# Kernel tuning notes

Measured on AMD Instinct MI355X. Metric: run time of the kernel, lower is better.

The kernel has to match this reference:

```python
import jax, jax.numpy as jnp
import numpy as np

EMBED_DIM = 1024
NUM_HEADS = 16
HEAD_DIM = EMBED_DIM // NUM_HEADS
SCALE_BASE = EMBED_DIM  # XPOS(head_dim, embed_dim): embed_dim is scale_base
BSZ, SEQ = 8, 1024


def xpos_apply(x, downscale):
    # x: [B*H, L, D]; standard xpos (torchscale) rotary with position-dependent scale
    L, D = x.shape[1], x.shape[2]
    half = D // 2
    s = (jnp.arange(0, D, 2, dtype=jnp.float32) + 0.4 * D) / (1.4 * D)  # [half]
    min_pos = -(L // 2)  # offset = 0
    pos = jnp.arange(min_pos, min_pos + L, dtype=jnp.float32)  # [L]
    scale = s[None, :] ** (pos[:, None] / SCALE_BASE)  # [L, half]
    inv_freq = 1.0 / (10000.0 ** (jnp.arange(half, dtype=jnp.float32) / half))
    sinus = jnp.arange(L, dtype=jnp.float32)[:, None] * inv_freq[None, :]  # [L, half]
    sin, cos = jnp.sin(sinus), jnp.cos(sinus)
    if downscale:
        scale = 1.0 / scale
    # duplicate_interleave: repeat each column twice -> [L, D]
    sin_d = jnp.repeat(sin * scale, 2, axis=-1)
    cos_d = jnp.repeat(cos * scale, 2, axis=-1)
    x1, x2 = x[..., 0::2], x[..., 1::2]
    rot = jnp.stack([-x2, x1], axis=-1).reshape(x.shape)  # rotate_every_two
    return x * cos_d + rot * sin_d


def setup_inputs() -> dict:
    key = jax.random.key(0)
    ks = jax.random.split(key, 12)
    std = 0.02
    inp = {
        'query': jax.random.normal(ks[0], (BSZ, SEQ, EMBED_DIM), jnp.float32),
        'key': jax.random.normal(ks[1], (BSZ, SEQ, EMBED_DIM), jnp.float32),
        'value': jax.random.normal(ks[2], (BSZ, SEQ, EMBED_DIM), jnp.float32),
        'wq': jax.random.normal(ks[3], (EMBED_DIM, EMBED_DIM), jnp.float32) * std,
        'bq': jax.random.normal(ks[4], (EMBED_DIM,), jnp.float32) * std,
        'wk': jax.random.normal(ks[5], (EMBED_DIM, EMBED_DIM), jnp.float32) * std,
        'bk': jax.random.normal(ks[6], (EMBED_DIM,), jnp.float32) * std,
        'wv': jax.random.normal(ks[7], (EMBED_DIM, EMBED_DIM), jnp.float32) * std,
        'bv': jax.random.normal(ks[8], (EMBED_DIM,), jnp.float32) * std,
        'wo': jax.random.normal(ks[9], (EMBED_DIM, EMBED_DIM), jnp.float32) * std,
        'bo': jax.random.normal(ks[10], (EMBED_DIM,), jnp.float32) * std,
    }
    return inp


def reference(query, key, value, wq, bq, wk, bk, wv, bv, wo, bo):
    B, T, E = query.shape
    S = key.shape[1]
    scaling = HEAD_DIM ** -0.5
    q = (query @ wq.T + bq) * scaling
    k = key @ wk.T + bk
    v = value @ wv.T + bv

    def split_heads(x, L):
        return x.reshape(B, L, NUM_HEADS, HEAD_DIM).transpose(0, 2, 1, 3).reshape(B * NUM_HEADS, L, HEAD_DIM)

    q = split_heads(q, T)
    k = split_heads(k, S)
    v = split_heads(v, S)
    k = xpos_apply(k, downscale=True)
    q = xpos_apply(q, downscale=False)
    attn_w = jnp.einsum('btd,bsd->bts', q, k)  # [B*H, T, S]
    attn_w = jax.nn.softmax(attn_w.astype(jnp.float32), axis=-1).astype(q.dtype)
    attn = jnp.einsum('bts,bsd->btd', attn_w, v)  # [B*H, T, D]
    attn = attn.reshape(B, NUM_HEADS, T, HEAD_DIM).transpose(0, 2, 1, 3).reshape(B, T, E)
    return attn @ wo.T + bo
```

## Files before the change

### kernel.cpp

```cpp
#include <hip/hip_runtime.h>


#define BSZ  8
#define SEQ  1024
#define EMB  1024
#define NH   16
#define HD   64
#define HALF 32
#define BH   (BSZ*NH)
#define MROWS (BSZ*SEQ)

typedef __attribute__((ext_vector_type(4))) float f32x4;
typedef __attribute__((ext_vector_type(8))) short bf16x8;

__device__ __forceinline__ ushort f2bf(float f) {
    union { float f; unsigned u; } v; v.f = f;
    return (ushort)((v.u + 0x7FFFu + ((v.u >> 16) & 1u)) >> 16);
}

__device__ __forceinline__ void async16(void* lds, const void* g) {
    __builtin_amdgcn_global_load_lds(
        (const __attribute__((address_space(1))) unsigned int*)g,
        (__attribute__((address_space(3))) unsigned int*)lds, 16, 0, 0);
}

__global__ __launch_bounds__(256)
void cast_kernel(const float* __restrict__ src, ushort* __restrict__ dst, int n4) {
    int i = blockIdx.x * 256 + threadIdx.x;
    if (i >= n4) return;
    float4 v = reinterpret_cast<const float4*>(src)[i];
    ushort4 o;
    o.x = f2bf(v.x); o.y = f2bf(v.y); o.z = f2bf(v.z); o.w = f2bf(v.w);
    reinterpret_cast<ushort4*>(dst)[i] = o;
}

__global__ __launch_bounds__(256)
void xpos_tables_kernel(float* __restrict__ tab) {
    int idx = blockIdx.x * 256 + threadIdx.x;
    if (idx >= SEQ * HALF) return;
    int t = idx >> 5;
    int j = idx & 31;
    float s        = (2.0f * (float)j + 0.4f * (float)HD) / (1.4f * (float)HD);
    float pos      = (float)(t - SEQ / 2);
    float scale    = powf(s, pos * (1.0f / 1024.0f));
    float inv_freq = powf(10000.0f, -(float)j / (float)HALF);
    float ang      = (float)t * inv_freq;
    float sn = sinf(ang), cs = cosf(ang);
    float inv_scale = 1.0f / scale;
    tab[0 * SEQ * HALF + idx] = sn * scale;
    tab[1 * SEQ * HALF + idx] = cs * scale;
    tab[2 * SEQ * HALF + idx] = sn * inv_scale;
    tab[3 * SEQ * HALF + idx] = cs * inv_scale;
}

template <int MODE>
__global__ __launch_bounds__(256)
void gemm_bf16_kernel(const ushort* __restrict__ A, const ushort* __restrict__ W,
                      const float* __restrict__ bias, const float* __restrict__ tab,
                      void* __restrict__ outp) {
    __shared__ ushort As[128 * 64];
    __shared__ ushort Bs[128 * 64];
    const int tid  = threadIdx.x;
    const int lane = tid & 63;
    const int w    = tid >> 6;
    const int g    = lane >> 4;
    const int c    = lane & 15;
    const int wr   = w >> 1, wc = w & 1;

    int lid = blockIdx.x;
    int wg  = (lid & 7) * 64 + (lid >> 3);
    const int row0 = (wg >> 3) * 128;
    const int col0 = (wg & 7) * 128;

    f32x4 acc[4][4] = {};

    int srow[4], scol[4];
    #pragma unroll
    for (int i = 0; i < 4; ++i) {
        int f = i * 4096 + tid * 16;
        int r = f >> 7, cb = f & 127;
        srow[i] = r;
        scol[i] = (cb ^ ((r & 7) << 4)) >> 1;
    }

    for (int k0 = 0; k0 < EMB; k0 += 64) {
        #pragma unroll
        for (int i = 0; i < 4; ++i) {
            const ushort* srcA;
            if (MODE == 3) {
                int h = k0 >> 6;
                srcA = &A[(((size_t)(row0 >> 10) * NH + h) * SEQ +
                           (row0 & 1023) + srow[i]) * HD + scol[i]];
            } else {
                srcA = &A[(size_t)(row0 + srow[i]) * EMB + k0 + scol[i]];
            }
            async16(&As[i * 2048 + w * 512], srcA);
        }
        #pragma unroll
        for (int i = 0; i < 4; ++i) {
            const ushort* srcB = &W[(size_t)(col0 + srow[i]) * EMB + k0 + scol[i]];
            async16(&Bs[i * 2048 + w * 512], srcB);
        }
        __syncthreads();

        #pragma unroll
        for (int ks = 0; ks < 2; ++ks) {
            bf16x8 af[4], bfr[4];
            #pragma unroll
            for (int mi = 0; mi < 4; ++mi) {
                int r = wr * 64 + mi * 16 + c;
                int byt = r * 128 + ((ks * 64 + g * 16) ^ ((r & 7) << 4));
                af[mi] = *reinterpret_cast<const bf16x8*>(
                    reinterpret_cast<const char*>(As) + byt);
            }
            #pragma unroll
            for (int ni = 0; ni < 4; ++ni) {
                int r = wc * 64 + ni * 16 + c;
                int byt = r * 128 + ((ks * 64 + g * 16) ^ ((r & 7) << 4));
                bfr[ni] = *reinterpret_cast<const bf16x8*>(
                    reinterpret_cast<const char*>(Bs) + byt);
            }
            #pragma unroll
            for (int mi = 0; mi < 4; ++mi)
                #pragma unroll
                for (int ni = 0; ni < 4; ++ni)
                    acc[mi][ni] = __builtin_amdgcn_mfma_f32_16x16x32_bf16(
                        af[mi], bfr[ni], acc[mi][ni], 0, 0, 0);
        }
        __syncthreads();
    }

    #pragma unroll
    for (int ni = 0; ni < 4; ++ni) {
        int n = col0 + wc * 64 + ni * 16 + c;
        float bn = bias[n];
        #pragma unroll
        for (int mi = 0; mi < 4; ++mi) {
            #pragma unroll
            for (int r = 0; r < 4; ++r) {
                int m = row0 + wr * 64 + mi * 16 + g * 4 + r;
                float val = acc[mi][ni][r] + bn;
                if (MODE == 1) val *= 0.125f;
                if (MODE == 1 || MODE == 2) {
                    int t = m & (SEQ - 1);
                    int d = n & 63;
                    const int base = (MODE == 1 ? 0 : 2) * SEQ * HALF + t * HALF;
                    float sn = tab[base + (d >> 1)];
                    float cs = tab[base + SEQ * HALF + (d >> 1)];
                    float other = __shfl_xor(val, 1);
                    val = val * cs + ((d & 1) ? other * sn : -other * sn);
                }
                if (MODE == 3) {
                    ((float*)outp)[(size_t)m * EMB + n] = val;
                } else {
                    int b = m >> 10, t = m & 1023;
                    int h = n >> 6,  d = n & 63;
                    ((ushort*)outp)[(((size_t)b * NH + h) * SEQ + t) * HD + d] =
                        f2bf(val);
                }
            }
        }
    }
}

__global__ __launch_bounds__(256)
void vtrans_kernel(const ushort* __restrict__ v, ushort* __restrict__ vt) {
    __shared__ ushort T[64][72];
    const int tid = threadIdx.x;
    const int bh  = blockIdx.y;
    const int t0  = blockIdx.x * 64;
    const ushort* vb = &v[((size_t)bh * SEQ + t0) * HD];
    #pragma unroll
    for (int p = 0; p < 2; ++p) {
        int chunk = p * 256 + tid;
        int tl = chunk >> 3;
        int d8 = (chunk & 7) * 8;
        ushort tmp[8];
        *reinterpret_cast<uint4*>(tmp) =
            *reinterpret_cast<const uint4*>(&vb[tl * HD + d8]);
        #pragma unroll
        for (int j = 0; j < 8; ++j) T[d8 + j][tl] = tmp[j];
    }
    __syncthreads();
    ushort* ob = &vt[(size_t)bh * HD * SEQ + t0];
    #pragma unroll
    for (int p = 0; p < 2; ++p) {
        int chunk = p * 256 + tid;
        int dl = chunk >> 3;
        int t8 = (chunk & 7) * 8;
        *reinterpret_cast<uint4*>(&ob[(size_t)dl * SEQ + t8]) =
            *reinterpret_cast<const uint4*>(&T[dl][t8]);
    }
}

__global__ __launch_bounds__(256)
void attn_kernel(const ushort* __restrict__ qg, const ushort* __restrict__ kg,
                 const ushort* __restrict__ vtg, ushort* __restrict__ og) {
    __shared__ ushort Ks[2 * 4096];
    __shared__ ushort Vs[2 * 4096];
    __shared__ ushort Ps[4096];
    const int tid  = threadIdx.x;
    const int lane = tid & 63;
    const int w    = tid >> 6;
    const int g    = lane >> 4;
    const int c    = lane & 15;

    int lid = blockIdx.x;
    int wg  = (lid & 7) * 256 + (lid >> 3);
    const int bh = wg >> 4;
    const int q0 = (wg & 15) * 64;

    const ushort* qrow = &qg[((size_t)bh * SEQ + q0 + w * 16 + c) * HD];
    bf16x8 qf[2];
    qf[0] = *reinterpret_cast<const bf16x8*>(qrow + g * 8);
    qf[1] = *reinterpret_cast<const bf16x8*>(qrow + 32 + g * 8);

    float m_i[4], l_i[4];
    f32x4 oacc[4] = {};
    #pragma unroll
    for (int r = 0; r < 4; ++r) { m_i[r] = -1e30f; l_i[r] = 0.f; }

    int srow[2], scol[2];
    #pragma unroll
    for (int i = 0; i < 2; ++i) {
        int f = i * 4096 + tid * 16;
        int r = f >> 7, cb = f & 127;
        srow[i] = r; scol[i] = (cb ^ ((r & 7) << 4)) >> 1;
    }

    const ushort* kb  = &kg[(size_t)bh * SEQ * HD];
    const ushort* vtb = &vtg[(size_t)bh * HD * SEQ];

    auto stage = [&](int buf, int kt) {
        #pragma unroll
        for (int i = 0; i < 2; ++i) {
            async16(&Ks[buf * 4096 + i * 2048 + w * 512],
                    &kb[(size_t)(kt + srow[i]) * HD + scol[i]]);
            async16(&Vs[buf * 4096 + i * 2048 + w * 512],
                    &vtb[(size_t)srow[i] * SEQ + kt + scol[i]]);
        }
    };

    stage(0, 0);
    __syncthreads();

    char* pbase = reinterpret_cast<char*>(Ps) + w * 2048;

    for (int kt = 0; kt < SEQ; kt += 64) {
        const int cur = (kt >> 6) & 1;
        if (kt + 64 < SEQ) stage(cur ^ 1, kt + 64);

        const char* kbase = reinterpret_cast<const char*>(Ks) + cur * 8192;
        const char* vbase = reinterpret_cast<const char*>(Vs) + cur * 8192;

        f32x4 s[4];
        #pragma unroll
        for (int j = 0; j < 4; ++j) {
            int key = j * 16 + c;
            int sw  = (key & 7) << 4;
            f32x4 a = {};
            #pragma unroll
            for (int ks = 0; ks < 2; ++ks) {
                bf16x8 kf = *reinterpret_cast<const bf16x8*>(
                    kbase + key * 128 + ((ks * 64 + g * 16) ^ sw));
                a = __builtin_amdgcn_mfma_f32_16x16x32_bf16(qf[ks], kf, a, 0, 0, 0);
            }
            s[j] = a;
        }

        float alpha[4];
        #pragma unroll
        for (int r = 0; r < 4; ++r) {
            float mx = fmaxf(fmaxf(s[0][r], s[1][r]), fmaxf(s[2][r], s[3][r]));
            mx = fmaxf(mx, __shfl_xor(mx, 1));
            mx = fmaxf(mx, __shfl_xor(mx, 2));
            mx = fmaxf(mx, __shfl_xor(mx, 4));
            mx = fmaxf(mx, __shfl_xor(mx, 8));
            float mn = fmaxf(m_i[r], mx);
            alpha[r] = __expf(m_i[r] - mn);
            float rs = 0.f;
            #pragma unroll
            for (int j = 0; j < 4; ++j) {
                float p = __expf(s[j][r] - mn);
                s[j][r] = p;
                rs += p;
            }
            rs += __shfl_xor(rs, 1);
            rs += __shfl_xor(rs, 2);
            rs += __shfl_xor(rs, 4);
            rs += __shfl_xor(rs, 8);
            l_i[r] = l_i[r] * alpha[r] + rs;
            m_i[r] = mn;
        }

        #pragma unroll
        for (int r = 0; r < 4; ++r) {
            int q  = g * 4 + r;
            int sw = (q & 7) << 4;
            #pragma unroll
            for (int j = 0; j < 4; ++j) {
                int byt = q * 128 + (((j * 16 + c) * 2) ^ sw);
                *reinterpret_cast<ushort*>(pbase + byt) = f2bf(s[j][r]);
            }
        }
        #pragma unroll
        for (int dblk = 0; dblk < 4; ++dblk)
            #pragma unroll
            for (int r = 0; r < 4; ++r)
                oacc[dblk][r] *= alpha[r];

        #pragma unroll
        for (int ks = 0; ks < 2; ++ks) {
            bf16x8 pf = *reinterpret_cast<const bf16x8*>(
                pbase + c * 128 + ((ks * 64 + g * 16) ^ ((c & 7) << 4)));
            #pragma unroll
            for (int dblk = 0; dblk < 4; ++dblk) {
                int d = dblk * 16 + c;
                bf16x8 vf = *reinterpret_cast<const bf16x8*>(
                    vbase + d * 128 + ((ks * 64 + g * 16) ^ ((d & 7) << 4)));
                oacc[dblk] = __builtin_amdgcn_mfma_f32_16x16x32_bf16(
                    pf, vf, oacc[dblk], 0, 0, 0);
            }
        }
        __syncthreads();
    }

    #pragma unroll
    for (int r = 0; r < 4; ++r) {
        float inv = 1.f / l_i[r];
        int q = q0 + w * 16 + g * 4 + r;
        #pragma unroll
        for (int dblk = 0; dblk < 4; ++dblk)
            og[((size_t)bh * SEQ + q) * HD + dblk * 16 + c] =
                f2bf(oacc[dblk][r] * inv);
    }
}

extern "C" void kernel_launch(void* const* d_in, const int* in_sizes, int n_in,
                              void* d_out, int out_size, void* d_ws,
                              size_t ws_size, hipStream_t stream) {
    const float* query = (const float*)d_in[0];
    const float* key_  = (const float*)d_in[1];
    const float* value = (const float*)d_in[2];
    const float* wq    = (const float*)d_in[3];
    const float* bq    = (const float*)d_in[4];
    const float* wk    = (const float*)d_in[5];
    const float* bk    = (const float*)d_in[6];
    const float* wv    = (const float*)d_in[7];
    const float* bv    = (const float*)d_in[8];
    const float* wo    = (const float*)d_in[9];
    const float* bo    = (const float*)d_in[10];

    ushort* ws16 = (ushort*)d_ws;
    const size_t NX = (size_t)MROWS * EMB;
    const size_t NW = (size_t)EMB * EMB;
    ushort* tmp = ws16;
    ushort* wqb = ws16 + NX;
    ushort* wkb = wqb + NW;
    ushort* wvb = wkb + NW;
    ushort* wob = wvb + NW;
    float*  tab = (float*)(wob + NW);
    ushort* qb  = (ushort*)(tab + 4 * SEQ * HALF);
    ushort* kb  = qb + NX;
    ushort* vb  = kb + NX;

    const int nx4 = (int)(NX / 4), nw4 = (int)(NW / 4);

    cast_kernel<<<nw4 / 256, 256, 0, stream>>>(wq, wqb, nw4);
    cast_kernel<<<nw4 / 256, 256, 0, stream>>>(wk, wkb, nw4);
    cast_kernel<<<nw4 / 256, 256, 0, stream>>>(wv, wvb, nw4);
    cast_kernel<<<nw4 / 256, 256, 0, stream>>>(wo, wob, nw4);
    xpos_tables_kernel<<<SEQ * HALF / 256, 256, 0, stream>>>(tab);

    cast_kernel<<<nx4 / 256, 256, 0, stream>>>(query, tmp, nx4);
    gemm_bf16_kernel<1><<<512, 256, 0, stream>>>(tmp, wqb, bq, tab, qb);
    cast_kernel<<<nx4 / 256, 256, 0, stream>>>(key_, tmp, nx4);
    gemm_bf16_kernel<2><<<512, 256, 0, stream>>>(tmp, wkb, bk, tab, kb);
    cast_kernel<<<nx4 / 256, 256, 0, stream>>>(value, tmp, nx4);
    gemm_bf16_kernel<0><<<512, 256, 0, stream>>>(tmp, wvb, bv, tab, vb);

    vtrans_kernel<<<dim3(16, 128), 256, 0, stream>>>(vb, tmp);

    attn_kernel<<<2048, 256, 0, stream>>>(qb, kb, tmp, vb);

    gemm_bf16_kernel<3><<<512, 256, 0, stream>>>(vb, wob, bo, nullptr, d_out);
}
```

Baseline: 391.5 us.

## Fuse input casts into batched QKV GEMM and add lazy softmax rescaling

The fp32-to-bf16 activation casts are folded into one QKV GEMM kernel that loads fp32 rows, converts them in registers and writes them to LDS. The three projections now run as a single launch over a y-dimension, and the four weight casts become one launch. This removes three full activation cast passes and several launches. In attention, the running max is only updated when a tile's max exceeds it by more than a threshold, and the row-sum shuffle reductions move out of the loop to the end. The trade-off is that the A operand no longer uses async LDS loads, so global-load latency is less hidden, and the lazy rescale relies on the exp values staying bounded.

```diff
diff --git a/kernel.cpp b/kernel.cpp
--- a/kernel.cpp
+++ b/kernel.cpp
@@ -12,6 +12,7 @@
 
 typedef __attribute__((ext_vector_type(4))) float f32x4;
 typedef __attribute__((ext_vector_type(8))) short bf16x8;
+typedef __attribute__((ext_vector_type(8))) unsigned short u16x8;
 
 __device__ __forceinline__ ushort f2bf(float f) {
     union { float f; unsigned u; } v; v.f = f;
@@ -25,13 +26,20 @@
 }
 
 __global__ __launch_bounds__(256)
-void cast_kernel(const float* __restrict__ src, ushort* __restrict__ dst, int n4) {
+void castw_kernel(const float* __restrict__ w0, const float* __restrict__ w1,
+                  const float* __restrict__ w2, const float* __restrict__ w3,
+                  ushort* __restrict__ d0, ushort* __restrict__ d1,
+                  ushort* __restrict__ d2, ushort* __restrict__ d3, int n4) {
     int i = blockIdx.x * 256 + threadIdx.x;
     if (i >= n4) return;
-    float4 v = reinterpret_cast<const float4*>(src)[i];
+    const float* s = blockIdx.y == 0 ? w0 : blockIdx.y == 1 ? w1
+                   : blockIdx.y == 2 ? w2 : w3;
+    ushort* d = blockIdx.y == 0 ? d0 : blockIdx.y == 1 ? d1
+              : blockIdx.y == 2 ? d2 : d3;
+    float4 v = reinterpret_cast<const float4*>(s)[i];
     ushort4 o;
     o.x = f2bf(v.x); o.y = f2bf(v.y); o.z = f2bf(v.z); o.w = f2bf(v.w);
-    reinterpret_cast<ushort4*>(dst)[i] = o;
+    reinterpret_cast<ushort4*>(d)[i] = o;
 }
 
 __global__ __launch_bounds__(256)
@@ -53,13 +61,24 @@
     tab[3 * SEQ * HALF + idx] = cs * inv_scale;
 }
 
-template <int MODE>
-__global__ __launch_bounds__(256)
-void gemm_bf16_kernel(const ushort* __restrict__ A, const ushort* __restrict__ W,
-                      const float* __restrict__ bias, const float* __restrict__ tab,
-                      void* __restrict__ outp) {
+__global__ __launch_bounds__(256)
+void qkv_gemm_kernel(const float* __restrict__ Aq, const float* __restrict__ Ak,
+                     const float* __restrict__ Av,
+                     const ushort* __restrict__ Wq, const ushort* __restrict__ Wk,
+                     const ushort* __restrict__ Wv,
+                     const float* __restrict__ bq, const float* __restrict__ bk,
+                     const float* __restrict__ bv,
+                     const float* __restrict__ tab,
+                     ushort* __restrict__ oq, ushort* __restrict__ ok,
+                     ushort* __restrict__ ov) {
     __shared__ ushort As[128 * 64];
     __shared__ ushort Bs[128 * 64];
+    const int ymode = blockIdx.y;
+    const float*  A    = ymode == 0 ? Aq : ymode == 1 ? Ak : Av;
+    const ushort* W    = ymode == 0 ? Wq : ymode == 1 ? Wk : Wv;
+    const float*  bias = ymode == 0 ? bq : ymode == 1 ? bk : bv;
+    ushort*       outp = ymode == 0 ? oq : ymode == 1 ? ok : ov;
+
     const int tid  = threadIdx.x;
     const int lane = tid & 63;
     const int w    = tid >> 6;
@@ -74,6 +93,10 @@
 
     f32x4 acc[4][4] = {};
 
+    const int ar  = tid >> 1;
+    const int ach = (tid & 1) * 32;
+    const int asw = (ar & 7) << 4;
+
     int srow[4], scol[4];
     #pragma unroll
     for (int i = 0; i < 4; ++i) {
@@ -84,23 +107,24 @@
     }
 
     for (int k0 = 0; k0 < EMB; k0 += 64) {
-        #pragma unroll
-        for (int i = 0; i < 4; ++i) {
-            const ushort* srcA;
-            if (MODE == 3) {
-                int h = k0 >> 6;
-                srcA = &A[(((size_t)(row0 >> 10) * NH + h) * SEQ +
-                           (row0 & 1023) + srow[i]) * HD + scol[i]];
-            } else {
-                srcA = &A[(size_t)(row0 + srow[i]) * EMB + k0 + scol[i]];
-            }
-            async16(&As[i * 2048 + w * 512], srcA);
-        }
-        #pragma unroll
-        for (int i = 0; i < 4; ++i) {
-            const ushort* srcB = &W[(size_t)(col0 + srow[i]) * EMB + k0 + scol[i]];
-            async16(&Bs[i * 2048 + w * 512], srcB);
-        }
+        const float4* asrc = reinterpret_cast<const float4*>(
+            &A[(size_t)(row0 + ar) * EMB + k0 + ach]);
+        float4 av[8];
+        #pragma unroll
+        for (int i = 0; i < 8; ++i) av[i] = asrc[i];
+        #pragma unroll
+        for (int a = 0; a < 4; ++a) {
+            u16x8 u;
+            const float* pf = reinterpret_cast<const float*>(&av[2 * a]);
+            #pragma unroll
+            for (int e = 0; e < 8; ++e) u[e] = f2bf(pf[e]);
+            int byt = ar * 128 + ((2 * (ach + 8 * a)) ^ asw);
+            *reinterpret_cast<u16x8*>(reinterpret_cast<char*>(As) + byt) = u;
+        }
+        #pragma unroll
+        for (int i = 0; i < 4; ++i)
+            async16(&Bs[i * 2048 + w * 512],
+                    &W[(size_t)(col0 + srow[i]) * EMB + k0 + scol[i]]);
         __syncthreads();
 
         #pragma unroll
@@ -140,24 +164,19 @@
             for (int r = 0; r < 4; ++r) {
                 int m = row0 + wr * 64 + mi * 16 + g * 4 + r;
                 float val = acc[mi][ni][r] + bn;
-                if (MODE == 1) val *= 0.125f;
-                if (MODE == 1 || MODE == 2) {
+                if (ymode == 0) val *= 0.125f;
+                if (ymode != 2) {
                     int t = m & (SEQ - 1);
                     int d = n & 63;
-                    const int base = (MODE == 1 ? 0 : 2) * SEQ * HALF + t * HALF;
+                    const int base = (ymode == 0 ? 0 : 2) * SEQ * HALF + t * HALF;
                     float sn = tab[base + (d >> 1)];
                     float cs = tab[base + SEQ * HALF + (d >> 1)];
                     float other = __shfl_xor(val, 1);
                     val = val * cs + ((d & 1) ? other * sn : -other * sn);
                 }
-                if (MODE == 3) {
-                    ((float*)outp)[(size_t)m * EMB + n] = val;
-                } else {
-                    int b = m >> 10, t = m & 1023;
-                    int h = n >> 6,  d = n & 63;
-                    ((ushort*)outp)[(((size_t)b * NH + h) * SEQ + t) * HD + d] =
-                        f2bf(val);
-                }
+                int b = m >> 10, t = m & 1023;
+                int h = n >> 6,  d = n & 63;
+                outp[(((size_t)b * NH + h) * SEQ + t) * HD + d] = f2bf(val);
             }
         }
     }
@@ -215,10 +234,10 @@
     qf[0] = *reinterpret_cast<const bf16x8*>(qrow + g * 8);
     qf[1] = *reinterpret_cast<const bf16x8*>(qrow + 32 + g * 8);
 
-    float m_i[4], l_i[4];
+    float m_run[4], l_part[4];
     f32x4 oacc[4] = {};
     #pragma unroll
-    for (int r = 0; r < 4; ++r) { m_i[r] = -1e30f; l_i[r] = 0.f; }
+    for (int r = 0; r < 4; ++r) { m_run[r] = -1e30f; l_part[r] = 0.f; }
 
     int srow[2], scol[2];
     #pragma unroll
@@ -268,29 +287,27 @@
             s[j] = a;
         }
 
-        float alpha[4];
-        #pragma unroll
-        for (int r = 0; r < 4; ++r) {
-            float mx = fmaxf(fmaxf(s[0][r], s[1][r]), fmaxf(s[2][r], s[3][r]));
-            mx = fmaxf(mx, __shfl_xor(mx, 1));
-            mx = fmaxf(mx, __shfl_xor(mx, 2));
-            mx = fmaxf(mx, __shfl_xor(mx, 4));
-            mx = fmaxf(mx, __shfl_xor(mx, 8));
-            float mn = fmaxf(m_i[r], mx);
-            alpha[r] = __expf(m_i[r] - mn);
-            float rs = 0.f;
-            #pragma unroll
-            for (int j = 0; j < 4; ++j) {
-                float p = __expf(s[j][r] - mn);
-                s[j][r] = p;
-                rs += p;
-            }
-            rs += __shfl_xor(rs, 1);
-            rs += __shfl_xor(rs, 2);
-            rs += __shfl_xor(rs, 4);
-            rs += __shfl_xor(rs, 8);
-            l_i[r] = l_i[r] * alpha[r] + rs;
-            m_i[r] = mn;
+        float pmax[4];
+        #pragma unroll
+        for (int r = 0; r < 4; ++r)
+            pmax[r] = fmaxf(fmaxf(s[0][r], s[1][r]), fmaxf(s[2][r], s[3][r]));
+        int need = (pmax[0] > m_run[0] + 8.f) || (pmax[1] > m_run[1] + 8.f) ||
+                   (pmax[2] > m_run[2] + 8.f) || (pmax[3] > m_run[3] + 8.f);
+        if (__any(need)) {
+            #pragma unroll
+            for (int r = 0; r < 4; ++r) {
+                float mx = pmax[r];
+                mx = fmaxf(mx, __shfl_xor(mx, 1));
+                mx = fmaxf(mx, __shfl_xor(mx, 2));
+                mx = fmaxf(mx, __shfl_xor(mx, 4));
+                mx = fmaxf(mx, __shfl_xor(mx, 8));
+                float mn = fmaxf(m_run[r], mx);
+                float alpha = __expf(m_run[r] - mn);
+                l_part[r] *= alpha;
+                #pragma unroll
+                for (int dblk = 0; dblk < 4; ++dblk) oacc[dblk][r] *= alpha;
+                m_run[r] = mn;
+            }
         }
 
         #pragma unroll
@@ -299,15 +316,12 @@
             int sw = (q & 7) << 4;
             #pragma unroll
             for (int j = 0; j < 4; ++j) {
+                float p = __expf(s[j][r] - m_run[r]);
+                l_part[r] += p;
                 int byt = q * 128 + (((j * 16 + c) * 2) ^ sw);
-                *reinterpret_cast<ushort*>(pbase + byt) = f2bf(s[j][r]);
-            }
-        }
-        #pragma unroll
-        for (int dblk = 0; dblk < 4; ++dblk)
-            #pragma unroll
-            for (int r = 0; r < 4; ++r)
-                oacc[dblk][r] *= alpha[r];
+                *reinterpret_cast<ushort*>(pbase + byt) = f2bf(p);
+            }
+        }
 
         #pragma unroll
         for (int ks = 0; ks < 2; ++ks) {
@@ -327,12 +341,100 @@
 
     #pragma unroll
     for (int r = 0; r < 4; ++r) {
-        float inv = 1.f / l_i[r];
+        float rs = l_part[r];
+        rs += __shfl_xor(rs, 1);
+        rs += __shfl_xor(rs, 2);
+        rs += __shfl_xor(rs, 4);
+        rs += __shfl_xor(rs, 8);
+        float inv = 1.f / rs;
         int q = q0 + w * 16 + g * 4 + r;
         #pragma unroll
         for (int dblk = 0; dblk < 4; ++dblk)
             og[((size_t)bh * SEQ + q) * HD + dblk * 16 + c] =
                 f2bf(oacc[dblk][r] * inv);
+    }
+}
+
+__global__ __launch_bounds__(256)
+void outproj_kernel(const ushort* __restrict__ A, const ushort* __restrict__ W,
+                    const float* __restrict__ bias, float* __restrict__ out) {
+    __shared__ ushort As[128 * 64];
+    __shared__ ushort Bs[128 * 64];
+    const int tid  = threadIdx.x;
+    const int lane = tid & 63;
+    const int w    = tid >> 6;
+    const int g    = lane >> 4;
+    const int c    = lane & 15;
+    const int wr   = w >> 1, wc = w & 1;
+
+    int lid = blockIdx.x;
+    int wg  = (lid & 7) * 64 + (lid >> 3);
+    const int row0 = (wg >> 3) * 128;
+    const int col0 = (wg & 7) * 128;
+
+    f32x4 acc[4][4] = {};
+
+    int srow[4], scol[4];
+    #pragma unroll
+    for (int i = 0; i < 4; ++i) {
+        int f = i * 4096 + tid * 16;
+        int r = f >> 7, cb = f & 127;
+        srow[i] = r;
+        scol[i] = (cb ^ ((r & 7) << 4)) >> 1;
+    }
+
+    for (int k0 = 0; k0 < EMB; k0 += 64) {
+        int h = k0 >> 6;
+        #pragma unroll
+        for (int i = 0; i < 4; ++i)
+            async16(&As[i * 2048 + w * 512],
+                    &A[(((size_t)(row0 >> 10) * NH + h) * SEQ +
+                        (row0 & 1023) + srow[i]) * HD + scol[i]]);
+        #pragma unroll
+        for (int i = 0; i < 4; ++i)
+            async16(&Bs[i * 2048 + w * 512],
+                    &W[(size_t)(col0 + srow[i]) * EMB + k0 + scol[i]]);
+        __syncthreads();
+
+        #pragma unroll
+        for (int ks = 0; ks < 2; ++ks) {
+            bf16x8 af[4], bfr[4];
+            #pragma unroll
+            for (int mi = 0; mi < 4; ++mi) {
+                int r = wr * 64 + mi * 16 + c;
+                int byt = r * 128 + ((ks * 64 + g * 16) ^ ((r & 7) << 4));
+                af[mi] = *reinterpret_cast<const bf16x8*>(
+                    reinterpret_cast<const char*>(As) + byt);
+            }
+            #pragma unroll
+            for (int ni = 0; ni < 4; ++ni) {
+                int r = wc * 64 + ni * 16 + c;
+                int byt = r * 128 + ((ks * 64 + g * 16) ^ ((r & 7) << 4));
+                bfr[ni] = *reinterpret_cast<const bf16x8*>(
+                    reinterpret_cast<const char*>(Bs) + byt);
+            }
+            #pragma unroll
+            for (int mi = 0; mi < 4; ++mi)
+                #pragma unroll
+                for (int ni = 0; ni < 4; ++ni)
+                    acc[mi][ni] = __builtin_amdgcn_mfma_f32_16x16x32_bf16(
+                        af[mi], bfr[ni], acc[mi][ni], 0, 0, 0);
+        }
+        __syncthreads();
+    }
+
+    #pragma unroll
+    for (int ni = 0; ni < 4; ++ni) {
+        int n = col0 + wc * 64 + ni * 16 + c;
+        float bn = bias[n];
+        #pragma unroll
+        for (int mi = 0; mi < 4; ++mi) {
+            #pragma unroll
+            for (int r = 0; r < 4; ++r) {
+                int m = row0 + wr * 64 + mi * 16 + g * 4 + r;
+                out[(size_t)m * EMB + n] = acc[mi][ni][r] + bn;
+            }
+        }
     }
 }
 
@@ -354,34 +456,27 @@
     ushort* ws16 = (ushort*)d_ws;
     const size_t NX = (size_t)MROWS * EMB;
     const size_t NW = (size_t)EMB * EMB;
-    ushort* tmp = ws16;
-    ushort* wqb = ws16 + NX;
+    ushort* qb  = ws16;
+    ushort* kb  = qb + NX;
+    ushort* vb  = kb + NX;
+    ushort* vt  = vb + NX;
+    ushort* wqb = vt + NX;
     ushort* wkb = wqb + NW;
     ushort* wvb = wkb + NW;
     ushort* wob = wvb + NW;
     float*  tab = (float*)(wob + NW);
-    ushort* qb  = (ushort*)(tab + 4 * SEQ * HALF);
-    ushort* kb  = qb + NX;
-    ushort* vb  = kb + NX;
-
-    const int nx4 = (int)(NX / 4), nw4 = (int)(NW / 4);
-
-    cast_kernel<<<nw4 / 256, 256, 0, stream>>>(wq, wqb, nw4);
-    cast_kernel<<<nw4 / 256, 256, 0, stream>>>(wk, wkb, nw4);
-    cast_kernel<<<nw4 / 256, 256, 0, stream>>>(wv, wvb, nw4);
-    cast_kernel<<<nw4 / 256, 256, 0, stream>>>(wo, wob, nw4);
+
+    const int nw4 = (int)(NW / 4);
+    castw_kernel<<<dim3(nw4 / 256, 4), 256, 0, stream>>>(
+        wq, wk, wv, wo, wqb, wkb, wvb, wob, nw4);
     xpos_tables_kernel<<<SEQ * HALF / 256, 256, 0, stream>>>(tab);
 
-    cast_kernel<<<nx4 / 256, 256, 0, stream>>>(query, tmp, nx4);
-    gemm_bf16_kernel<1><<<512, 256, 0, stream>>>(tmp, wqb, bq, tab, qb);
-    cast_kernel<<<nx4 / 256, 256, 0, stream>>>(key_, tmp, nx4);
-    gemm_bf16_kernel<2><<<512, 256, 0, stream>>>(tmp, wkb, bk, tab, kb);
-    cast_kernel<<<nx4 / 256, 256, 0, stream>>>(value, tmp, nx4);
-    gemm_bf16_kernel<0><<<512, 256, 0, stream>>>(tmp, wvb, bv, tab, vb);
-
-    vtrans_kernel<<<dim3(16, 128), 256, 0, stream>>>(vb, tmp);
-
-    attn_kernel<<<2048, 256, 0, stream>>>(qb, kb, tmp, vb);
-
-    gemm_bf16_kernel<3><<<512, 256, 0, stream>>>(vb, wob, bo, nullptr, d_out);
-}
+    qkv_gemm_kernel<<<dim3(512, 3), 256, 0, stream>>>(
+        query, key_, value, wqb, wkb, wvb, bq, bk, bv, tab, qb, kb, vb);
+
+    vtrans_kernel<<<dim3(16, 128), 256, 0, stream>>>(vb, vt);
+
+    attn_kernel<<<2048, 256, 0, stream>>>(qb, kb, vt, vb);
+
+    outproj_kernel<<<512, 256, 0, stream>>>(vb, wob, bo, (float*)d_out);
+}
```

After: 428.5 us. +9.4%, slower.

## Double-buffer GEMM tiles, lazy softmax rescale in attention, merge weight casts

Applied to the files above, without the earlier changes.

The GEMM kernel now double-buffers its A/B LDS tiles, issuing the async loads for the next k-slice before computing on the current one, so global latency overlaps with MFMA work. The attention kernel adopts a lazy online-softmax: it rescales the accumulators only when some row max exceeds the running max by more than 8, keeps per-lane partial row sums, and reduces them once at the end. The four weight cast launches are merged into one 2D launch. The GEMM doubles its LDS use (64KB), which may lower occupancy, and the single sync per iteration with the prefetch in flight relies on the barrier ordering being right.

```diff
diff --git a/kernel.cpp b/kernel.cpp
--- a/kernel.cpp
+++ b/kernel.cpp
@@ -32,6 +32,23 @@
     ushort4 o;
     o.x = f2bf(v.x); o.y = f2bf(v.y); o.z = f2bf(v.z); o.w = f2bf(v.w);
     reinterpret_cast<ushort4*>(dst)[i] = o;
+}
+
+__global__ __launch_bounds__(256)
+void castw_kernel(const float* __restrict__ w0, const float* __restrict__ w1,
+                  const float* __restrict__ w2, const float* __restrict__ w3,
+                  ushort* __restrict__ d0, ushort* __restrict__ d1,
+                  ushort* __restrict__ d2, ushort* __restrict__ d3, int n4) {
+    int i = blockIdx.x * 256 + threadIdx.x;
+    if (i >= n4) return;
+    const float* s = blockIdx.y == 0 ? w0 : blockIdx.y == 1 ? w1
+                   : blockIdx.y == 2 ? w2 : w3;
+    ushort* d = blockIdx.y == 0 ? d0 : blockIdx.y == 1 ? d1
+              : blockIdx.y == 2 ? d2 : d3;
+    float4 v = reinterpret_cast<const float4*>(s)[i];
+    ushort4 o;
+    o.x = f2bf(v.x); o.y = f2bf(v.y); o.z = f2bf(v.z); o.w = f2bf(v.w);
+    reinterpret_cast<ushort4*>(d)[i] = o;
 }
 
 __global__ __launch_bounds__(256)
@@ -58,8 +75,8 @@
 void gemm_bf16_kernel(const ushort* __restrict__ A, const ushort* __restrict__ W,
                       const float* __restrict__ bias, const float* __restrict__ tab,
                       void* __restrict__ outp) {
-    __shared__ ushort As[128 * 64];
-    __shared__ ushort Bs[128 * 64];
+    __shared__ ushort As[2][128 * 64];
+    __shared__ ushort Bs[2][128 * 64];
     const int tid  = threadIdx.x;
     const int lane = tid & 63;
     const int w    = tid >> 6;
@@ -83,7 +100,7 @@
         scol[i] = (cb ^ ((r & 7) << 4)) >> 1;
     }
 
-    for (int k0 = 0; k0 < EMB; k0 += 64) {
+    auto stage = [&](int buf, int k0) {
         #pragma unroll
         for (int i = 0; i < 4; ++i) {
             const ushort* srcA;
@@ -94,31 +111,37 @@
             } else {
                 srcA = &A[(size_t)(row0 + srow[i]) * EMB + k0 + scol[i]];
             }
-            async16(&As[i * 2048 + w * 512], srcA);
-        }
-        #pragma unroll
-        for (int i = 0; i < 4; ++i) {
-            const ushort* srcB = &W[(size_t)(col0 + srow[i]) * EMB + k0 + scol[i]];
-            async16(&Bs[i * 2048 + w * 512], srcB);
-        }
-        __syncthreads();
-
+            async16(&As[buf][i * 2048 + w * 512], srcA);
+        }
+        #pragma unroll
+        for (int i = 0; i < 4; ++i)
+            async16(&Bs[buf][i * 2048 + w * 512],
+                    &W[(size_t)(col0 + srow[i]) * EMB + k0 + scol[i]]);
+    };
+
+    stage(0, 0);
+    __syncthreads();
+
+    for (int t = 0; t < 16; ++t) {
+        const int cur = t & 1;
+        if (t < 15) stage(cur ^ 1, (t + 1) * 64);
+
+        const char* abase = reinterpret_cast<const char*>(As[cur]);
+        const char* bbase = reinterpret_cast<const char*>(Bs[cur]);
         #pragma unroll
         for (int ks = 0; ks < 2; ++ks) {
             bf16x8 af[4], bfr[4];
             #pragma unroll
             for (int mi = 0; mi < 4; ++mi) {
                 int r = wr * 64 + mi * 16 + c;
-                int byt = r * 128 + ((ks * 64 + g * 16) ^ ((r & 7) << 4));
                 af[mi] = *reinterpret_cast<const bf16x8*>(
-                    reinterpret_cast<const char*>(As) + byt);
+                    abase + r * 128 + ((ks * 64 + g * 16) ^ ((r & 7) << 4)));
             }
             #pragma unroll
             for (int ni = 0; ni < 4; ++ni) {
                 int r = wc * 64 + ni * 16 + c;
-                int byt = r * 128 + ((ks * 64 + g * 16) ^ ((r & 7) << 4));
                 bfr[ni] = *reinterpret_cast<const bf16x8*>(
-                    reinterpret_cast<const char*>(Bs) + byt);
+                    bbase + r * 128 + ((ks * 64 + g * 16) ^ ((r & 7) << 4)));
             }
             #pragma unroll
             for (int mi = 0; mi < 4; ++mi)
@@ -215,10 +238,10 @@
     qf[0] = *reinterpret_cast<const bf16x8*>(qrow + g * 8);
     qf[1] = *reinterpret_cast<const bf16x8*>(qrow + 32 + g * 8);
 
-    float m_i[4], l_i[4];
+    float m_run[4], l_part[4];
     f32x4 oacc[4] = {};
     #pragma unroll
-    for (int r = 0; r < 4; ++r) { m_i[r] = -1e30f; l_i[r] = 0.f; }
+    for (int r = 0; r < 4; ++r) { m_run[r] = -1e30f; l_part[r] = 0.f; }
 
     int srow[2], scol[2];
     #pragma unroll
@@ -268,29 +291,27 @@
             s[j] = a;
         }
 
-        float alpha[4];
-        #pragma unroll
-        for (int r = 0; r < 4; ++r) {
-            float mx = fmaxf(fmaxf(s[0][r], s[1][r]), fmaxf(s[2][r], s[3][r]));
-            mx = fmaxf(mx, __shfl_xor(mx, 1));
-            mx = fmaxf(mx, __shfl_xor(mx, 2));
-            mx = fmaxf(mx, __shfl_xor(mx, 4));
-            mx = fmaxf(mx, __shfl_xor(mx, 8));
-            float mn = fmaxf(m_i[r], mx);
-            alpha[r] = __expf(m_i[r] - mn);
-            float rs = 0.f;
-            #pragma unroll
-            for (int j = 0; j < 4; ++j) {
-                float p = __expf(s[j][r] - mn);
-                s[j][r] = p;
-                rs += p;
-            }
-            rs += __shfl_xor(rs, 1);
-            rs += __shfl_xor(rs, 2);
-            rs += __shfl_xor(rs, 4);
-            rs += __shfl_xor(rs, 8);
-            l_i[r] = l_i[r] * alpha[r] + rs;
-            m_i[r] = mn;
+        float pmax[4];
+        #pragma unroll
+        for (int r = 0; r < 4; ++r)
+            pmax[r] = fmaxf(fmaxf(s[0][r], s[1][r]), fmaxf(s[2][r], s[3][r]));
+        int need = (pmax[0] > m_run[0] + 8.f) || (pmax[1] > m_run[1] + 8.f) ||
+                   (pmax[2] > m_run[2] + 8.f) || (pmax[3] > m_run[3] + 8.f);
+        if (__any(need)) {
+            #pragma unroll
+            for (int r = 0; r < 4; ++r) {
+                float mx = pmax[r];
+                mx = fmaxf(mx, __shfl_xor(mx, 1));
+                mx = fmaxf(mx, __shfl_xor(mx, 2));
+                mx = fmaxf(mx, __shfl_xor(mx, 4));
+                mx = fmaxf(mx, __shfl_xor(mx, 8));
+                float mn = fmaxf(m_run[r], mx);
+                float alpha = __expf(m_run[r] - mn);
+                l_part[r] *= alpha;
+                #pragma unroll
+                for (int dblk = 0; dblk < 4; ++dblk) oacc[dblk][r] *= alpha;
+                m_run[r] = mn;
+            }
         }
 
         #pragma unroll
@@ -299,15 +320,12 @@
             int sw = (q & 7) << 4;
             #pragma unroll
             for (int j = 0; j < 4; ++j) {
+                float p = __expf(s[j][r] - m_run[r]);
+                l_part[r] += p;
                 int byt = q * 128 + (((j * 16 + c) * 2) ^ sw);
-                *reinterpret_cast<ushort*>(pbase + byt) = f2bf(s[j][r]);
-            }
-        }
-        #pragma unroll
-        for (int dblk = 0; dblk < 4; ++dblk)
-            #pragma unroll
-            for (int r = 0; r < 4; ++r)
-                oacc[dblk][r] *= alpha[r];
+                *reinterpret_cast<ushort*>(pbase + byt) = f2bf(p);
+            }
+        }
 
         #pragma unroll
         for (int ks = 0; ks < 2; ++ks) {
@@ -327,7 +345,12 @@
 
     #pragma unroll
     for (int r = 0; r < 4; ++r) {
-        float inv = 1.f / l_i[r];
+        float rs = l_part[r];
+        rs += __shfl_xor(rs, 1);
+        rs += __shfl_xor(rs, 2);
+        rs += __shfl_xor(rs, 4);
+        rs += __shfl_xor(rs, 8);
+        float inv = 1.f / rs;
         int q = q0 + w * 16 + g * 4 + r;
         #pragma unroll
         for (int dblk = 0; dblk < 4; ++dblk)
@@ -366,10 +389,8 @@
 
     const int nx4 = (int)(NX / 4), nw4 = (int)(NW / 4);
 
-    cast_kernel<<<nw4 / 256, 256, 0, stream>>>(wq, wqb, nw4);
-    cast_kernel<<<nw4 / 256, 256, 0, stream>>>(wk, wkb, nw4);
-    cast_kernel<<<nw4 / 256, 256, 0, stream>>>(wv, wvb, nw4);
-    cast_kernel<<<nw4 / 256, 256, 0, stream>>>(wo, wob, nw4);
+    castw_kernel<<<dim3(nw4 / 256, 4), 256, 0, stream>>>(
+        wq, wk, wv, wo, wqb, wkb, wvb, wob, nw4);
     xpos_tables_kernel<<<SEQ * HALF / 256, 256, 0, stream>>>(tab);
 
     cast_kernel<<<nx4 / 256, 256, 0, stream>>>(query, tmp, nx4);
@@ -383,5 +404,6 @@
 
     attn_kernel<<<2048, 256, 0, stream>>>(qb, kb, tmp, vb);
 
-    gemm_bf16_kernel<3><<<512, 256, 0, stream>>>(vb, wob, bo, nullptr, d_out);
-}
+    gemm_bf16_kernel<3><<<512, 256, 0, stream>>>(vb, wob, bo, nullptr,
+                                                 (float*)d_out);
+}
```

New measurement: 352.4 us. 1.11x faster.
